# Performance work log

Measured on AMD Instinct MI355X. Metric: run time of the kernel, lower is better.

The kernel has to match this reference:

```python
import jax, jax.numpy as jnp
import numpy as np
from jax import lax

B = 32768        # batch
L = 1024         # input_size
K = 5            # kernel_size
PAD = K - 1      # circular padding = 4
FEA = L + (PAD - K // 2) * 2   # mem_fea_dim = 1028
MEM_DIM = 50
DATE_DIM = 32
SHRINK = 0.0025
EPS = 1e-12
DN = ('NCH', 'OIH', 'NCH')


def setup_inputs() -> dict:
    key = jax.random.key(0)
    ks = jax.random.split(key, 10)
    s = 0.05
    return {
        'x': jax.random.normal(ks[0], (B, L), jnp.float32),
        'date_vector': jax.random.normal(ks[1], (B, DATE_DIM), jnp.float32),
        'conv_w': jax.random.normal(ks[2], (1, 1, K), jnp.float32) * s,    # Conv1d weight [out,in,k]
        'convt_w': jax.random.normal(ks[3], (1, 1, K), jnp.float32) * s,   # ConvTranspose1d weight
        'mem_W': jax.random.normal(ks[4], (MEM_DIM, FEA), jnp.float32) * s,      # memory bank (codebook)
        'date_W': jax.random.normal(ks[5], (MEM_DIM, DATE_DIM), jnp.float32) * s, # date addressing weights
        'fcw_w': jax.random.normal(ks[6], (1, L), jnp.float32) * s,
        'fcw_b': jnp.zeros((1,), jnp.float32),
        'fcb_w': jax.random.normal(ks[7], (1, L), jnp.float32) * s,
        'fcb_b': jnp.zeros((1,), jnp.float32),
    }


def _forward(x, date_vector, conv_w, convt_w, mem_W, date_W, fcw_w, fcw_b, fcb_w, fcb_b):
    # --- encode: 1-channel circular conv (bias forced to 0 in original forward) ---
    st = x[:, None, :]                                            # [B,1,L]
    stp = jnp.pad(st, ((0, 0), (0, 0), (PAD, PAD)), mode='wrap')  # circular pad
    st = lax.conv_general_dilated(stp, conv_w, (1,), 'VALID', dimension_numbers=DN)  # [B,1,FEA]

    # --- DateMemoryUnit: date-addressed read with hard shrink + L1 renorm ---
    scores = date_vector @ date_W.T                               # [B,MEM_DIM]
    att = jax.nn.softmax(scores, axis=-1)
    att = jax.nn.relu(att - SHRINK) * att / (jnp.abs(att - SHRINK) + EPS)
    att = att / (jnp.sum(jnp.abs(att), axis=-1, keepdims=True) + EPS)
    st_mem = att @ mem_W                                          # [B,FEA]
    st = st_mem.reshape(B, 1, FEA)

    # --- decode: ConvTranspose1d(k=5, stride=1, padding=4) == VALID conv with flipped kernel ---
    st = lax.conv_general_dilated(st, jnp.flip(convt_w, -1), (1,), 'VALID', dimension_numbers=DN)
    st = st[:, 0, :]                                              # [B,L]

    # --- trend blend ---
    mtf = 0.5
    weight = jnp.tanh(x @ fcw_w.T + fcw_b) * mtf + 1.0            # [B,1]
    bias = jnp.tanh(x @ fcb_w.T + fcb_b) * mtf                    # [B,1]
    st = st * weight + bias
    return st, weight, bias


def reference(x, date_vector, conv_w, convt_w, mem_W, date_W, fcw_w, fcw_b, fcb_w, fcb_b):
    return _forward(x, date_vector, conv_w, convt_w, mem_W, date_W, fcw_w, fcw_b, fcb_w, fcb_b)
```

## Files before the change

kernel.cpp:

```cpp
#include <hip/hip_runtime.h>
#include <hip/hip_bf16.h>

#define BB   32768
#define LL   1024
#define FEA  1028
#define MEM  50
#define DATE 32

typedef float  f32x4  __attribute__((ext_vector_type(4)));
typedef __bf16 bf16x8 __attribute__((ext_vector_type(8)));

__device__ __forceinline__ float wave_max(float v) {
    #pragma unroll
    for (int off = 32; off; off >>= 1) v = fmaxf(v, __shfl_xor(v, off));
    return v;
}
__device__ __forceinline__ float wave_sum(float v) {
    #pragma unroll
    for (int off = 32; off; off >>= 1) v += __shfl_xor(v, off);
    return v;
}

__global__ void prep_wc(const float* __restrict__ convt_w,
                        const float* __restrict__ mem_W,
                        __bf16* __restrict__ wc) {
    int idx = blockIdx.x * 256 + threadIdx.x;
    int i = idx >> 6, k = idx & 63;
    float acc = 0.f;
    if (k < MEM) {
        #pragma unroll
        for (int j = 0; j < 5; ++j)
            acc += convt_w[j] * mem_W[k * FEA + i + 4 - j];
    }
    wc[i * 64 + k] = (__bf16)acc;
}

__global__ __launch_bounds__(256) void memconv_main(
        const float* __restrict__ x,
        const float* __restrict__ dv,
        const float* __restrict__ dW,
        const float* __restrict__ fcw_w, const float* __restrict__ fcw_b,
        const float* __restrict__ fcb_w, const float* __restrict__ fcb_b,
        const __bf16* __restrict__ wc,
        float* __restrict__ out) {
    __shared__ __bf16 att_s[32 * 72];
    __shared__ float  w_s[32], b_s[32];

    const int tid  = threadIdx.x;
    const int lane = tid & 63;
    const int wid  = tid >> 6;
    const int b0   = blockIdx.x * 32;

    {
        int m = lane < MEM ? lane : MEM - 1;
        float dwv[DATE];
        const f32x4* dwp = (const f32x4*)(dW + m * DATE);
        #pragma unroll
        for (int c = 0; c < 8; ++c) {
            f32x4 v = dwp[c];
            #pragma unroll
            for (int j = 0; j < 4; ++j) dwv[c * 4 + j] = v[j];
        }
        for (int rr = 0; rr < 8; ++rr) {
            int r = wid * 8 + rr;
            int b = b0 + r;
            const f32x4* dvp = (const f32x4*)(dv + (size_t)b * DATE);
            float sc = 0.f;
            #pragma unroll
            for (int c = 0; c < 8; ++c) {
                f32x4 v = dvp[c];
                #pragma unroll
                for (int j = 0; j < 4; ++j) sc += v[j] * dwv[c * 4 + j];
            }
            float scm = (lane < MEM) ? sc : -1e30f;
            float mx  = wave_max(scm);
            float e   = (lane < MEM) ? __expf(sc - mx) : 0.f;
            float s   = wave_sum(e);
            float p   = e / s;
            float d   = p - 0.0025f;
            float p2  = (d > 0.f) ? p * d / (d + 1e-12f) : 0.f;
            float s2  = wave_sum(p2) + 1e-12f;
            float att = p2 / s2;
            att_s[r * 72 + lane] = (lane < MEM) ? (__bf16)att : (__bf16)0.f;
        }
    }

    {
        const int cg = lane & 15;
        const int rg = lane >> 4;
        #pragma unroll
        for (int g = 0; g < 2; ++g) {
            int r = wid * 8 + g * 4 + rg;
            int b = b0 + r;
            float aw = 0.f, ab = 0.f;
            #pragma unroll
            for (int c = 0; c < 16; ++c) {
                int off = cg * 4 + c * 64;
                f32x4 xv = *(const f32x4*)(x + (size_t)b * LL + off);
                f32x4 wv = *(const f32x4*)(fcw_w + off);
                f32x4 bv = *(const f32x4*)(fcb_w + off);
                #pragma unroll
                for (int j = 0; j < 4; ++j) {
                    aw += xv[j] * wv[j];
                    ab += xv[j] * bv[j];
                }
            }
            #pragma unroll
            for (int off = 1; off <= 8; off <<= 1) {
                aw += __shfl_xor(aw, off);
                ab += __shfl_xor(ab, off);
            }
            if (cg == 0) {
                float w  = tanhf(aw + fcw_b[0]) * 0.5f + 1.0f;
                float bi = tanhf(ab + fcb_b[0]) * 0.5f;
                w_s[r] = w; b_s[r] = bi;
                out[(size_t)BB * LL + b]      = w;
                out[(size_t)BB * LL + BB + b] = bi;
            }
        }
    }
    __syncthreads();

    {
        const int cg = lane & 15;
        const int kg = lane >> 4;
        bf16x8 a[2][2];
        #pragma unroll
        for (int rt = 0; rt < 2; ++rt) {
            int r = rt * 16 + cg;
            a[rt][0] = *(const bf16x8*)(att_s + r * 72 + kg * 8);
            a[rt][1] = *(const bf16x8*)(att_s + r * 72 + kg * 8 + 32);
        }
        float wreg[8], breg[8];
        #pragma unroll
        for (int rt = 0; rt < 2; ++rt)
            #pragma unroll
            for (int r4 = 0; r4 < 4; ++r4) {
                int row = rt * 16 + kg * 4 + r4;
                wreg[rt * 4 + r4] = w_s[row];
                breg[rt * 4 + r4] = b_s[row];
            }
        for (int nt = 0; nt < 16; ++nt) {
            int nc = wid * 256 + nt * 16;
            int n  = nc + cg;
            bf16x8 bf0 = *(const bf16x8*)(wc + n * 64 + kg * 8);
            bf16x8 bf1 = *(const bf16x8*)(wc + n * 64 + kg * 8 + 32);
            #pragma unroll
            for (int rt = 0; rt < 2; ++rt) {
                f32x4 acc = {0.f, 0.f, 0.f, 0.f};
                acc = __builtin_amdgcn_mfma_f32_16x16x32_bf16(a[rt][0], bf0, acc, 0, 0, 0);
                acc = __builtin_amdgcn_mfma_f32_16x16x32_bf16(a[rt][1], bf1, acc, 0, 0, 0);
                #pragma unroll
                for (int r4 = 0; r4 < 4; ++r4) {
                    int row = rt * 16 + kg * 4 + r4;
                    float v = acc[r4] * wreg[rt * 4 + r4] + breg[rt * 4 + r4];
                    out[(size_t)(b0 + row) * LL + n] = v;
                }
            }
        }
    }
}

extern "C" void kernel_launch(void* const* d_in, const int* in_sizes, int n_in,
                              void* d_out, int out_size, void* d_ws, size_t ws_size,
                              hipStream_t stream) {
    const float* x     = (const float*)d_in[0];
    const float* dv    = (const float*)d_in[1];
    const float* convt = (const float*)d_in[3];
    const float* memW  = (const float*)d_in[4];
    const float* dateW = (const float*)d_in[5];
    const float* fcww  = (const float*)d_in[6];
    const float* fcwb  = (const float*)d_in[7];
    const float* fcbw  = (const float*)d_in[8];
    const float* fcbb  = (const float*)d_in[9];
    float* out = (float*)d_out;
    __bf16* wc = (__bf16*)d_ws;

    prep_wc<<<256, 256, 0, stream>>>(convt, memW, wc);
    memconv_main<<<BB / 32, 256, 0, stream>>>(x, dv, dateW, fcww, fcwb, fcbw, fcbb, wc, out);
}
```

Baseline: 279.2 us.

## Split fused kernel into attention, fc, and swapped-operand GEMM epilogue kernels

Breaks the single fused kernel into separate kernels for the attention softmax, the fc weight/bias reductions, and the MFMA GEMM with epilogue, passing attention and weight/bias through global workspace. The GEMM swaps the A/B operands so each lane holds four consecutive output columns, which allows 16-byte vector stores instead of scalar column-strided stores, and it launches four times as many blocks. This targets the store inefficiency and the low parallelism of the write-bound output path. The cost is extra launches and a global round trip for the attention and weight/bias data.

```diff
diff --git a/kernel.cpp b/kernel.cpp
--- a/kernel.cpp
+++ b/kernel.cpp
@@ -25,138 +25,139 @@
                         const float* __restrict__ mem_W,
                         __bf16* __restrict__ wc) {
     int idx = blockIdx.x * 256 + threadIdx.x;
-    int i = idx >> 6, k = idx & 63;
+    int n = idx >> 6, k = idx & 63;
     float acc = 0.f;
     if (k < MEM) {
         #pragma unroll
         for (int j = 0; j < 5; ++j)
-            acc += convt_w[j] * mem_W[k * FEA + i + 4 - j];
+            acc += convt_w[j] * mem_W[k * FEA + n + 4 - j];
     }
-    wc[i * 64 + k] = (__bf16)acc;
+    wc[n * 64 + k] = (__bf16)acc;
 }
 
-__global__ __launch_bounds__(256) void memconv_main(
+__global__ __launch_bounds__(256) void att_kernel(
+        const float* __restrict__ dv, const float* __restrict__ dW,
+        __bf16* __restrict__ att_g) {
+    const int lane = threadIdx.x & 63;
+    const int wid  = threadIdx.x >> 6;
+    int m = lane < MEM ? lane : MEM - 1;
+    float dwv[DATE];
+    const f32x4* dwp = (const f32x4*)(dW + m * DATE);
+    #pragma unroll
+    for (int c = 0; c < 8; ++c) {
+        f32x4 v = dwp[c];
+        #pragma unroll
+        for (int j = 0; j < 4; ++j) dwv[c * 4 + j] = v[j];
+    }
+    for (int rr = 0; rr < 8; ++rr) {
+        int b = blockIdx.x * 32 + wid * 8 + rr;
+        const f32x4* dvp = (const f32x4*)(dv + (size_t)b * DATE);
+        float sc = 0.f;
+        #pragma unroll
+        for (int c = 0; c < 8; ++c) {
+            f32x4 v = dvp[c];
+            #pragma unroll
+            for (int j = 0; j < 4; ++j) sc += v[j] * dwv[c * 4 + j];
+        }
+        float scm = (lane < MEM) ? sc : -1e30f;
+        float mx  = wave_max(scm);
+        float e   = (lane < MEM) ? __expf(sc - mx) : 0.f;
+        float s   = wave_sum(e);
+        float p   = e / s;
+        float d   = p - 0.0025f;
+        float p2  = (d > 0.f) ? p * d / (d + 1e-12f) : 0.f;
+        float s2  = wave_sum(p2) + 1e-12f;
+        float att = p2 / s2;
+        att_g[(size_t)b * 64 + lane] = (lane < MEM) ? (__bf16)att : (__bf16)0.f;
+    }
+}
+
+__global__ __launch_bounds__(256) void fc_wb(
         const float* __restrict__ x,
-        const float* __restrict__ dv,
-        const float* __restrict__ dW,
         const float* __restrict__ fcw_w, const float* __restrict__ fcw_b,
         const float* __restrict__ fcb_w, const float* __restrict__ fcb_b,
-        const __bf16* __restrict__ wc,
-        float* __restrict__ out) {
-    __shared__ __bf16 att_s[32 * 72];
-    __shared__ float  w_s[32], b_s[32];
-
-    const int tid  = threadIdx.x;
-    const int lane = tid & 63;
-    const int wid  = tid >> 6;
-    const int b0   = blockIdx.x * 32;
-
-    {
-        int m = lane < MEM ? lane : MEM - 1;
-        float dwv[DATE];
-        const f32x4* dwp = (const f32x4*)(dW + m * DATE);
+        float* __restrict__ outtail) {
+    const int lane = threadIdx.x & 63;
+    const int wid  = threadIdx.x >> 6;
+    const int r0   = blockIdx.x * 16 + wid * 4;
+    f32x4 wv[4], bv[4];
+    #pragma unroll
+    for (int i = 0; i < 4; ++i) {
+        int c = i * 256 + lane * 4;
+        wv[i] = *(const f32x4*)(fcw_w + c);
+        bv[i] = *(const f32x4*)(fcb_w + c);
+    }
+    f32x4 xv[4][4];
+    #pragma unroll
+    for (int r = 0; r < 4; ++r)
         #pragma unroll
-        for (int c = 0; c < 8; ++c) {
-            f32x4 v = dwp[c];
+        for (int i = 0; i < 4; ++i)
+            xv[r][i] = *(const f32x4*)(x + (size_t)(r0 + r) * LL + i * 256 + lane * 4);
+    #pragma unroll
+    for (int r = 0; r < 4; ++r) {
+        float aw = 0.f, ab = 0.f;
+        #pragma unroll
+        for (int i = 0; i < 4; ++i)
             #pragma unroll
-            for (int j = 0; j < 4; ++j) dwv[c * 4 + j] = v[j];
+            for (int j = 0; j < 4; ++j) {
+                aw += xv[r][i][j] * wv[i][j];
+                ab += xv[r][i][j] * bv[i][j];
+            }
+        #pragma unroll
+        for (int off = 1; off <= 32; off <<= 1) {
+            aw += __shfl_xor(aw, off);
+            ab += __shfl_xor(ab, off);
         }
-        for (int rr = 0; rr < 8; ++rr) {
-            int r = wid * 8 + rr;
-            int b = b0 + r;
-            const f32x4* dvp = (const f32x4*)(dv + (size_t)b * DATE);
-            float sc = 0.f;
-            #pragma unroll
-            for (int c = 0; c < 8; ++c) {
-                f32x4 v = dvp[c];
-                #pragma unroll
-                for (int j = 0; j < 4; ++j) sc += v[j] * dwv[c * 4 + j];
-            }
-            float scm = (lane < MEM) ? sc : -1e30f;
-            float mx  = wave_max(scm);
-            float e   = (lane < MEM) ? __expf(sc - mx) : 0.f;
-            float s   = wave_sum(e);
-            float p   = e / s;
-            float d   = p - 0.0025f;
-            float p2  = (d > 0.f) ? p * d / (d + 1e-12f) : 0.f;
-            float s2  = wave_sum(p2) + 1e-12f;
-            float att = p2 / s2;
-            att_s[r * 72 + lane] = (lane < MEM) ? (__bf16)att : (__bf16)0.f;
+        if (lane == 0) {
+            outtail[r0 + r]      = tanhf(aw + fcw_b[0]) * 0.5f + 1.0f;
+            outtail[BB + r0 + r] = tanhf(ab + fcb_b[0]) * 0.5f;
         }
     }
+}
 
-    {
-        const int cg = lane & 15;
-        const int rg = lane >> 4;
+__global__ __launch_bounds__(256) void gemm_ep(
+        const __bf16* __restrict__ att_g, const __bf16* __restrict__ wc,
+        const float* __restrict__ wb, float* __restrict__ out) {
+    const int lane = threadIdx.x & 63;
+    const int wid  = threadIdx.x >> 6;
+    const int cg   = lane & 15;
+    const int kg   = lane >> 4;
+    const int bc   = blockIdx.x & 3;
+    const int br   = blockIdx.x >> 2;
+    const int b0   = br * 32;
+    const int n0   = bc * 256 + wid * 64;
+
+    bf16x8 bfr[2][2];
+    #pragma unroll
+    for (int ct = 0; ct < 2; ++ct)
         #pragma unroll
-        for (int g = 0; g < 2; ++g) {
-            int r = wid * 8 + g * 4 + rg;
-            int b = b0 + r;
-            float aw = 0.f, ab = 0.f;
+        for (int h = 0; h < 2; ++h)
+            bfr[ct][h] = *(const bf16x8*)(att_g + (size_t)(b0 + ct * 16 + cg) * 64 + h * 32 + kg * 8);
+
+    float wreg[2], breg[2];
+    #pragma unroll
+    for (int ct = 0; ct < 2; ++ct) {
+        int b = b0 + ct * 16 + cg;
+        wreg[ct] = wb[b];
+        breg[ct] = wb[BB + b];
+    }
+
+    #pragma unroll
+    for (int nt = 0; nt < 4; ++nt) {
+        int n = n0 + nt * 16 + cg;
+        bf16x8 a0 = *(const bf16x8*)(wc + n * 64 + kg * 8);
+        bf16x8 a1 = *(const bf16x8*)(wc + n * 64 + 32 + kg * 8);
+        #pragma unroll
+        for (int ct = 0; ct < 2; ++ct) {
+            f32x4 acc = {0.f, 0.f, 0.f, 0.f};
+            acc = __builtin_amdgcn_mfma_f32_16x16x32_bf16(a0, bfr[ct][0], acc, 0, 0, 0);
+            acc = __builtin_amdgcn_mfma_f32_16x16x32_bf16(a1, bfr[ct][1], acc, 0, 0, 0);
+            f32x4 v;
             #pragma unroll
-            for (int c = 0; c < 16; ++c) {
-                int off = cg * 4 + c * 64;
-                f32x4 xv = *(const f32x4*)(x + (size_t)b * LL + off);
-                f32x4 wv = *(const f32x4*)(fcw_w + off);
-                f32x4 bv = *(const f32x4*)(fcb_w + off);
-                #pragma unroll
-                for (int j = 0; j < 4; ++j) {
-                    aw += xv[j] * wv[j];
-                    ab += xv[j] * bv[j];
-                }
-            }
-            #pragma unroll
-            for (int off = 1; off <= 8; off <<= 1) {
-                aw += __shfl_xor(aw, off);
-                ab += __shfl_xor(ab, off);
-            }
-            if (cg == 0) {
-                float w  = tanhf(aw + fcw_b[0]) * 0.5f + 1.0f;
-                float bi = tanhf(ab + fcb_b[0]) * 0.5f;
-                w_s[r] = w; b_s[r] = bi;
-                out[(size_t)BB * LL + b]      = w;
-                out[(size_t)BB * LL + BB + b] = bi;
-            }
-        }
-    }
-    __syncthreads();
-
-    {
-        const int cg = lane & 15;
-        const int kg = lane >> 4;
-        bf16x8 a[2][2];
-        #pragma unroll
-        for (int rt = 0; rt < 2; ++rt) {
-            int r = rt * 16 + cg;
-            a[rt][0] = *(const bf16x8*)(att_s + r * 72 + kg * 8);
-            a[rt][1] = *(const bf16x8*)(att_s + r * 72 + kg * 8 + 32);
-        }
-        float wreg[8], breg[8];
-        #pragma unroll
-        for (int rt = 0; rt < 2; ++rt)
-            #pragma unroll
-            for (int r4 = 0; r4 < 4; ++r4) {
-                int row = rt * 16 + kg * 4 + r4;
-                wreg[rt * 4 + r4] = w_s[row];
-                breg[rt * 4 + r4] = b_s[row];
-            }
-        for (int nt = 0; nt < 16; ++nt) {
-            int nc = wid * 256 + nt * 16;
-            int n  = nc + cg;
-            bf16x8 bf0 = *(const bf16x8*)(wc + n * 64 + kg * 8);
-            bf16x8 bf1 = *(const bf16x8*)(wc + n * 64 + kg * 8 + 32);
-            #pragma unroll
-            for (int rt = 0; rt < 2; ++rt) {
-                f32x4 acc = {0.f, 0.f, 0.f, 0.f};
-                acc = __builtin_amdgcn_mfma_f32_16x16x32_bf16(a[rt][0], bf0, acc, 0, 0, 0);
-                acc = __builtin_amdgcn_mfma_f32_16x16x32_bf16(a[rt][1], bf1, acc, 0, 0, 0);
-                #pragma unroll
-                for (int r4 = 0; r4 < 4; ++r4) {
-                    int row = rt * 16 + kg * 4 + r4;
-                    float v = acc[r4] * wreg[rt * 4 + r4] + breg[rt * 4 + r4];
-                    out[(size_t)(b0 + row) * LL + n] = v;
-                }
-            }
+            for (int r4 = 0; r4 < 4; ++r4)
+                v[r4] = acc[r4] * wreg[ct] + breg[ct];
+            int brow = b0 + ct * 16 + cg;
+            *(f32x4*)(out + (size_t)brow * LL + n0 + nt * 16 + kg * 4) = v;
         }
     }
 }
@@ -174,8 +175,13 @@
     const float* fcbw  = (const float*)d_in[8];
     const float* fcbb  = (const float*)d_in[9];
     float* out = (float*)d_out;
-    __bf16* wc = (__bf16*)d_ws;
 
-    prep_wc<<<256, 256, 0, stream>>>(convt, memW, wc);
-    memconv_main<<<BB / 32, 256, 0, stream>>>(x, dv, dateW, fcww, fcwb, fcbw, fcbb, wc, out);
+    __bf16* wc    = (__bf16*)d_ws;
+    __bf16* att_g = (__bf16*)((char*)d_ws + 131072);
+    float*  outtail = out + (size_t)BB * LL;
+
+    prep_wc  <<<256,      256, 0, stream>>>(convt, memW, wc);
+    att_kernel<<<BB / 32, 256, 0, stream>>>(dv, dateW, att_g);
+    fc_wb    <<<BB / 16,  256, 0, stream>>>(x, fcww, fcwb, fcbw, fcbb, outtail);
+    gemm_ep  <<<(BB / 32) * 4, 256, 0, stream>>>(att_g, wc, outtail, out);
 }
```

New measurement: 289.0 us. +3.5%, slower.

## Swap MFMA operand roles for vectorized row stores and halve rows per block

Applied to the files above, without the earlier changes.

The MFMA operands are swapped so the codebook tile is the A operand and the attention rows are the B operand. Each lane now holds four consecutive output columns of one batch row and writes them with a single 16-byte store, replacing four scattered scalar stores. Rows per block drop from 32 to 16, which doubles the grid size and re-reads the wc tile twice as often per output row. The aim is to coalesce the dominant output write traffic, at the cost of more blocks and more wc loads.

```diff
diff --git a/kernel.cpp b/kernel.cpp
--- a/kernel.cpp
+++ b/kernel.cpp
@@ -25,17 +25,17 @@
                         const float* __restrict__ mem_W,
                         __bf16* __restrict__ wc) {
     int idx = blockIdx.x * 256 + threadIdx.x;
-    int i = idx >> 6, k = idx & 63;
+    int n = idx >> 6, k = idx & 63;
     float acc = 0.f;
     if (k < MEM) {
         #pragma unroll
         for (int j = 0; j < 5; ++j)
-            acc += convt_w[j] * mem_W[k * FEA + i + 4 - j];
+            acc += convt_w[j] * mem_W[k * FEA + n + 4 - j];
     }
-    wc[i * 64 + k] = (__bf16)acc;
+    wc[n * 64 + k] = (__bf16)acc;
 }
 
-__global__ __launch_bounds__(256) void memconv_main(
+__global__ __launch_bounds__(256) void memconv_fused(
         const float* __restrict__ x,
         const float* __restrict__ dv,
         const float* __restrict__ dW,
@@ -43,13 +43,14 @@
         const float* __restrict__ fcb_w, const float* __restrict__ fcb_b,
         const __bf16* __restrict__ wc,
         float* __restrict__ out) {
-    __shared__ __bf16 att_s[32 * 72];
-    __shared__ float  w_s[32], b_s[32];
+    __shared__ __bf16 att_s[16 * 80];
+    __shared__ float  w_s[16], b_s[16];
 
-    const int tid  = threadIdx.x;
-    const int lane = tid & 63;
-    const int wid  = tid >> 6;
-    const int b0   = blockIdx.x * 32;
+    const int lane = threadIdx.x & 63;
+    const int wid  = threadIdx.x >> 6;
+    const int cg   = lane & 15;
+    const int kg   = lane >> 4;
+    const int b0   = blockIdx.x * 16;
 
     {
         int m = lane < MEM ? lane : MEM - 1;
@@ -61,8 +62,9 @@
             #pragma unroll
             for (int j = 0; j < 4; ++j) dwv[c * 4 + j] = v[j];
         }
-        for (int rr = 0; rr < 8; ++rr) {
-            int r = wid * 8 + rr;
+        #pragma unroll
+        for (int rr = 0; rr < 4; ++rr) {
+            int r = wid * 4 + rr;
             int b = b0 + r;
             const f32x4* dvp = (const f32x4*)(dv + (size_t)b * DATE);
             float sc = 0.f;
@@ -81,82 +83,59 @@
             float p2  = (d > 0.f) ? p * d / (d + 1e-12f) : 0.f;
             float s2  = wave_sum(p2) + 1e-12f;
             float att = p2 / s2;
-            att_s[r * 72 + lane] = (lane < MEM) ? (__bf16)att : (__bf16)0.f;
+            att_s[r * 80 + lane] = (lane < MEM) ? (__bf16)att : (__bf16)0.f;
         }
     }
 
     {
-        const int cg = lane & 15;
-        const int rg = lane >> 4;
+        int r = wid * 4 + kg;
+        int b = b0 + r;
+        float aw = 0.f, ab = 0.f;
         #pragma unroll
-        for (int g = 0; g < 2; ++g) {
-            int r = wid * 8 + g * 4 + rg;
-            int b = b0 + r;
-            float aw = 0.f, ab = 0.f;
+        for (int c = 0; c < 16; ++c) {
+            int off = c * 64 + cg * 4;
+            f32x4 xv = *(const f32x4*)(x + (size_t)b * LL + off);
+            f32x4 wv = *(const f32x4*)(fcw_w + off);
+            f32x4 bv = *(const f32x4*)(fcb_w + off);
             #pragma unroll
-            for (int c = 0; c < 16; ++c) {
-                int off = cg * 4 + c * 64;
-                f32x4 xv = *(const f32x4*)(x + (size_t)b * LL + off);
-                f32x4 wv = *(const f32x4*)(fcw_w + off);
-                f32x4 bv = *(const f32x4*)(fcb_w + off);
-                #pragma unroll
-                for (int j = 0; j < 4; ++j) {
-                    aw += xv[j] * wv[j];
-                    ab += xv[j] * bv[j];
-                }
+            for (int j = 0; j < 4; ++j) {
+                aw += xv[j] * wv[j];
+                ab += xv[j] * bv[j];
             }
-            #pragma unroll
-            for (int off = 1; off <= 8; off <<= 1) {
-                aw += __shfl_xor(aw, off);
-                ab += __shfl_xor(ab, off);
-            }
-            if (cg == 0) {
-                float w  = tanhf(aw + fcw_b[0]) * 0.5f + 1.0f;
-                float bi = tanhf(ab + fcb_b[0]) * 0.5f;
-                w_s[r] = w; b_s[r] = bi;
-                out[(size_t)BB * LL + b]      = w;
-                out[(size_t)BB * LL + BB + b] = bi;
-            }
+        }
+        #pragma unroll
+        for (int off = 1; off <= 8; off <<= 1) {
+            aw += __shfl_xor(aw, off);
+            ab += __shfl_xor(ab, off);
+        }
+        if (cg == 0) {
+            float w  = tanhf(aw + fcw_b[0]) * 0.5f + 1.0f;
+            float bi = tanhf(ab + fcb_b[0]) * 0.5f;
+            w_s[r] = w; b_s[r] = bi;
+            out[(size_t)BB * LL + b]      = w;
+            out[(size_t)BB * LL + BB + b] = bi;
         }
     }
     __syncthreads();
 
     {
-        const int cg = lane & 15;
-        const int kg = lane >> 4;
-        bf16x8 a[2][2];
+        bf16x8 bfr0 = *(const bf16x8*)(att_s + cg * 80 + kg * 8);
+        bf16x8 bfr1 = *(const bf16x8*)(att_s + cg * 80 + 32 + kg * 8);
+        float wreg = w_s[cg], breg = b_s[cg];
+        float* orow = out + (size_t)(b0 + cg) * LL + wid * 256 + kg * 4;
+        const __bf16* wbase = wc + (wid * 256 + cg) * 64 + kg * 8;
         #pragma unroll
-        for (int rt = 0; rt < 2; ++rt) {
-            int r = rt * 16 + cg;
-            a[rt][0] = *(const bf16x8*)(att_s + r * 72 + kg * 8);
-            a[rt][1] = *(const bf16x8*)(att_s + r * 72 + kg * 8 + 32);
-        }
-        float wreg[8], breg[8];
-        #pragma unroll
-        for (int rt = 0; rt < 2; ++rt)
+        for (int nt = 0; nt < 16; ++nt) {
+            bf16x8 a0 = *(const bf16x8*)(wbase + nt * 16 * 64);
+            bf16x8 a1 = *(const bf16x8*)(wbase + nt * 16 * 64 + 32);
+            f32x4 acc = {0.f, 0.f, 0.f, 0.f};
+            acc = __builtin_amdgcn_mfma_f32_16x16x32_bf16(a0, bfr0, acc, 0, 0, 0);
+            acc = __builtin_amdgcn_mfma_f32_16x16x32_bf16(a1, bfr1, acc, 0, 0, 0);
+            f32x4 v;
             #pragma unroll
-            for (int r4 = 0; r4 < 4; ++r4) {
-                int row = rt * 16 + kg * 4 + r4;
-                wreg[rt * 4 + r4] = w_s[row];
-                breg[rt * 4 + r4] = b_s[row];
-            }
-        for (int nt = 0; nt < 16; ++nt) {
-            int nc = wid * 256 + nt * 16;
-            int n  = nc + cg;
-            bf16x8 bf0 = *(const bf16x8*)(wc + n * 64 + kg * 8);
-            bf16x8 bf1 = *(const bf16x8*)(wc + n * 64 + kg * 8 + 32);
-            #pragma unroll
-            for (int rt = 0; rt < 2; ++rt) {
-                f32x4 acc = {0.f, 0.f, 0.f, 0.f};
-                acc = __builtin_amdgcn_mfma_f32_16x16x32_bf16(a[rt][0], bf0, acc, 0, 0, 0);
-                acc = __builtin_amdgcn_mfma_f32_16x16x32_bf16(a[rt][1], bf1, acc, 0, 0, 0);
-                #pragma unroll
-                for (int r4 = 0; r4 < 4; ++r4) {
-                    int row = rt * 16 + kg * 4 + r4;
-                    float v = acc[r4] * wreg[rt * 4 + r4] + breg[rt * 4 + r4];
-                    out[(size_t)(b0 + row) * LL + n] = v;
-                }
-            }
+            for (int r4 = 0; r4 < 4; ++r4)
+                v[r4] = acc[r4] * wreg + breg;
+            *(f32x4*)(orow + nt * 16) = v;
         }
     }
 }
@@ -176,6 +155,6 @@
     float* out = (float*)d_out;
     __bf16* wc = (__bf16*)d_ws;
 
-    prep_wc<<<256, 256, 0, stream>>>(convt, memW, wc);
-    memconv_main<<<BB / 32, 256, 0, stream>>>(x, dv, dateW, fcww, fcwb, fcbw, fcbb, wc, out);
+    prep_wc      <<<256,     256, 0, stream>>>(convt, memW, wc);
+    memconv_fused<<<BB / 16, 256, 0, stream>>>(x, dv, dateW, fcww, fcwb, fcbw, fcbb, wc, out);
 }
```

Measured after the change: 285.7 us. 1.02x slower.
